# Kernel optimization log

Measured on AMD Instinct MI355X. Metric: run time of the kernel, lower is better.

The kernel has to match this reference:

```python
import jax, jax.numpy as jnp
import numpy as np
import math

B, S, D, H, R = 4, 2048, 512, 8, 8  # R = k+1 relative slots per direction


def setup_inputs() -> dict:
    key = jax.random.key(0)
    ks = jax.random.split(key, 16)
    dk = D // H
    sc = 1.0 / math.sqrt(D)
    return {
        "query": jax.random.normal(ks[0], (B, S, D), jnp.float32),
        "key": jax.random.normal(ks[1], (B, S, D), jnp.float32),
        "value": jax.random.normal(ks[2], (B, S, D), jnp.float32),
        "start_nodes": jax.random.randint(ks[3], (B, H, R, S), 0, S, jnp.int64 if jax.config.jax_enable_x64 else jnp.int32),
        "end_nodes": jax.random.randint(ks[4], (B, H, R, S), 0, S, jnp.int64 if jax.config.jax_enable_x64 else jnp.int32),
        "rel_q": jax.random.normal(ks[5], (1, H, 2 * R, dk), jnp.float32),
        "rel_k": jax.random.normal(ks[6], (1, H, 2 * R, dk), jnp.float32),
        "rel_v": jax.random.normal(ks[7], (1, H, 2 * R, dk), jnp.float32),
        "Wq": jax.random.normal(ks[8], (D, D), jnp.float32) * sc,
        "bq": jnp.zeros((D,), jnp.float32),
        "Wk": jax.random.normal(ks[9], (D, D), jnp.float32) * sc,
        "bk": jnp.zeros((D,), jnp.float32),
        "Wv": jax.random.normal(ks[10], (D, D), jnp.float32) * sc,
        "bv": jnp.zeros((D,), jnp.float32),
        "Wo": jax.random.normal(ks[11], (D, D), jnp.float32) * sc,
        "bo": jnp.zeros((D,), jnp.float32),
    }


def reference(query, key, value, start_nodes, end_nodes, rel_q, rel_k, rel_v,
              Wq, bq, Wk, bk, Wv, bv, Wo, bo):
    Bs, Ss, Ds = query.shape
    Hs = start_nodes.shape[1]
    dk = Ds // Hs

    def proj(x, W, b):
        return (x @ W.T + b).reshape(Bs, Ss, Hs, dk).transpose(0, 2, 1, 3)  # [B,H,S,dk]

    q = proj(query, Wq, bq)
    k = proj(key, Wk, bk)
    v = proj(value, Wv, bv)

    start_mask = start_nodes == -1
    sn = jnp.where(start_mask, 0, start_nodes)  # -1 padding -> 0 (masked out below)
    qidx = jnp.concatenate([end_nodes, sn], axis=2)  # [B,H,2R,S]
    kidx = jnp.concatenate([sn, end_nodes], axis=2)

    bi = jnp.arange(Bs)[:, None, None, None]
    hi = jnp.arange(Hs)[None, :, None, None]
    q_ctx = q[bi, hi, qidx]  # [B,H,2R,S,dk]
    k_ctx = k[bi, hi, kidx]
    v_ctx = v[bi, hi, kidx]

    # c2c + c2p + p2c, scale_factor = 3 (rel_q and rel_k both provided)
    scores = ((q_ctx * k_ctx).sum(-1)
              + (q_ctx * rel_k[:, :, :, None, :]).sum(-1)
              + (rel_q[:, :, :, None, :] * k_ctx).sum(-1))
    scores = scores / (3.0 * jnp.sqrt(jnp.asarray(dk, scores.dtype)))

    # mask: padded edges masked in both halves; first S flat entries always masked
    mask = jnp.concatenate([start_mask, start_mask], axis=2).reshape(Bs, Hs, -1)
    mask = mask.at[:, :, :Ss].set(True)
    sflat = jnp.exp(jnp.where(mask, -1e9, scores.reshape(Bs, Hs, -1)))  # [B,H,2R*S]

    qf = qidx.reshape(Bs, Hs, -1)
    b2 = jnp.arange(Bs)[:, None, None]
    h2 = jnp.arange(Hs)[None, :, None]
    # scatter-add softmax denominator over destination nodes, then gather back
    denom = jnp.zeros((Bs, Hs, Ss), sflat.dtype).at[b2, h2, qf].add(sflat)
    denom = jnp.where(denom == 0, -1e9, denom)
    probs = (sflat / denom[b2, h2, qf]).reshape(Bs, Hs, -1, Ss, 1)  # [B,H,2R,S,1]

    attn_v = probs * (v_ctx + rel_v[:, :, :, None, :])  # [B,H,2R,S,dk]
    out = jnp.zeros((Bs, Hs, Ss, dk), attn_v.dtype).at[b2, h2, qf].add(
        attn_v.reshape(Bs, Hs, -1, dk))  # scatter-add aggregation over edges

    out = out.transpose(0, 2, 1, 3).reshape(Bs, Ss, Ds)
    return out @ Wo.T + bo
```

## Files before the change

kernel.cpp:

```cpp
#include <hip/hip_runtime.h>
#include <math.h>

#define B_ 4
#define S_ 2048
#define D_ 512
#define H_ 8
#define R_ 8
#define DK_ 64
#define NEDGE (B_*H_*2*R_*S_)
#define EPB   (2*R_*S_)
#define ELLCAP 64
#define ELLSTRIDE 72
#define SCALE_ (1.0f/24.0f)

typedef __attribute__((ext_vector_type(8))) short bf16x8;
typedef __attribute__((ext_vector_type(8))) unsigned short ushort8_t;
typedef __attribute__((ext_vector_type(4))) float f32x4;

#define AS1q const __attribute__((address_space(1)))
#define AS3q __attribute__((address_space(3)))

__device__ inline unsigned short f2bf(float f) {
    unsigned u = __builtin_bit_cast(unsigned, f);
    u += 0x7fffu + ((u >> 16) & 1u);
    return (unsigned short)(u >> 16);
}
__device__ inline float bf2f(unsigned short u) {
    return __builtin_bit_cast(float, ((unsigned)u) << 16);
}

__global__ __launch_bounds__(256) void prep(
    const float* __restrict__ query, const float* __restrict__ key,
    const float* __restrict__ value,
    const float* __restrict__ Wq, const float* __restrict__ Wk,
    const float* __restrict__ Wv, const float* __restrict__ Wo,
    unsigned short* __restrict__ qc, unsigned short* __restrict__ kc,
    unsigned short* __restrict__ vc,
    unsigned short* __restrict__ wqb, unsigned short* __restrict__ wkb,
    unsigned short* __restrict__ wvb, unsigned short* __restrict__ wob)
{
    int bid = blockIdx.x;
    const float* x;
    unsigned short* y;
    size_t i;
    if (bid < 12288) {
        int z = bid >> 12;
        x = (z == 0) ? query : (z == 1) ? key : value;
        y = (z == 0) ? qc : (z == 1) ? kc : vc;
        i = ((size_t)(bid & 4095) * 256 + threadIdx.x) * 4;
    } else {
        int r = bid - 12288;
        int z = r >> 8;
        x = (z == 0) ? Wq : (z == 1) ? Wk : (z == 2) ? Wv : Wo;
        y = (z == 0) ? wqb : (z == 1) ? wkb : (z == 2) ? wvb : wob;
        i = ((size_t)(r & 255) * 256 + threadIdx.x) * 4;
    }
    float4 v = *(const float4*)&x[i];
    *(ushort4*)&y[i] = make_ushort4(f2bf(v.x), f2bf(v.y), f2bf(v.z), f2bf(v.w));
}

template<int TN>
__global__ __launch_bounds__(256) void gemm_bf16(
    const unsigned short* __restrict__ A0, const unsigned short* __restrict__ A1,
    const unsigned short* __restrict__ A2,
    const unsigned short* __restrict__ W0, const unsigned short* __restrict__ W1,
    const unsigned short* __restrict__ W2,
    const float* __restrict__ bi0, const float* __restrict__ bi1, const float* __restrict__ bi2,
    unsigned short* __restrict__ C0, unsigned short* __restrict__ C1,
    unsigned short* __restrict__ C2,
    float* __restrict__ Cf, int a_bhsd)
{
    constexpr int NFR = TN / 32;
    __shared__ unsigned short As[128 * 64];
    __shared__ unsigned short Bs[TN * 64];
    const int z = blockIdx.z;
    const unsigned short* A = (z == 0) ? A0 : (z == 1) ? A1 : A2;
    const unsigned short* W = (z == 0) ? W0 : (z == 1) ? W1 : W2;
    const float* bias        = (z == 0) ? bi0 : (z == 1) ? bi1 : bi2;
    unsigned short* C        = (z == 0) ? C0 : (z == 1) ? C1 : C2;

    const int t    = threadIdx.x;
    const int lane = t & 63;
    const int w    = t >> 6;
    const int wm   = w >> 1, wn = w & 1;
    const int m0   = blockIdx.x * 128;
    const int n0   = blockIdx.y * TN;

    const int lr    = lane >> 3;
    const int cglob = (lane & 7) ^ lr;

    f32x4 acc[4][NFR] = {};

    for (int kk = 0; kk < D_; kk += 64) {
        #pragma unroll
        for (int i = 0; i < 4; ++i) {
            int rowl = w * 32 + i * 8;
            int m = m0 + rowl + lr;
            const unsigned short* ga;
            if (a_bhsd) {
                int b = m >> 11, s = m & (S_ - 1), h = kk >> 6;
                ga = A + ((((size_t)b * H_ + h) * S_ + s) << 6) + cglob * 8;
            } else {
                ga = A + (size_t)m * D_ + kk + cglob * 8;
            }
            __builtin_amdgcn_global_load_lds((AS1q unsigned*)ga,
                (AS3q unsigned*)(As + rowl * 64), 16, 0, 0);
        }
        #pragma unroll
        for (int i = 0; i < TN / 32; ++i) {
            int rowl = w * (TN / 4) + i * 8;
            const unsigned short* gb =
                W + (size_t)(n0 + rowl + lr) * D_ + kk + cglob * 8;
            __builtin_amdgcn_global_load_lds((AS1q unsigned*)gb,
                (AS3q unsigned*)(Bs + rowl * 64), 16, 0, 0);
        }
        __syncthreads();

        #pragma unroll
        for (int ks = 0; ks < 64; ks += 32) {
            const int c0 = ks >> 3;
            bf16x8 af[4], bfr[NFR];
            #pragma unroll
            for (int mi = 0; mi < 4; ++mi) {
                int row = wm * 64 + mi * 16 + (lane & 15);
                int cp  = (c0 + (lane >> 4)) ^ (lane & 7);
                af[mi] = *(const bf16x8*)&As[row * 64 + cp * 8];
            }
            #pragma unroll
            for (int nj = 0; nj < NFR; ++nj) {
                int row = wn * (TN / 2) + nj * 16 + (lane & 15);
                int cp  = (c0 + (lane >> 4)) ^ (lane & 7);
                bfr[nj] = *(const bf16x8*)&Bs[row * 64 + cp * 8];
            }
            #pragma unroll
            for (int mi = 0; mi < 4; ++mi)
                #pragma unroll
                for (int nj = 0; nj < NFR; ++nj)
                    acc[mi][nj] = __builtin_amdgcn_mfma_f32_16x16x32_bf16(af[mi], bfr[nj], acc[mi][nj], 0, 0, 0);
        }
        __syncthreads();
    }

    #pragma unroll
    for (int mi = 0; mi < 4; ++mi) {
        #pragma unroll
        for (int nj = 0; nj < NFR; ++nj) {
            #pragma unroll
            for (int r = 0; r < 4; ++r) {
                int m = m0 + wm * 64 + mi * 16 + (lane >> 4) * 4 + r;
                int n = n0 + wn * (TN / 2) + nj * 16 + (lane & 15);
                float val = acc[mi][nj][r] + bias[n];
                if (Cf) {
                    Cf[(size_t)m * D_ + n] = val;
                } else {
                    int b = m >> 11, s = m & (S_ - 1);
                    int h = n >> 6,  d = n & 63;
                    C[((((size_t)b * H_ + h) * S_ + s) << 6) + d] = f2bf(val);
                }
            }
        }
    }
}

__global__ __launch_bounds__(256) void rel_dots(
    const unsigned short* __restrict__ q, const unsigned short* __restrict__ k_,
    const float* __restrict__ rel_q, const float* __restrict__ rel_k,
    float* __restrict__ qrk, float* __restrict__ rqk)
{
    const int t    = threadIdx.x;
    const int lane = t & 63;
    const int w    = t >> 6;
    const int n0   = blockIdx.x * 128 + w * 32;
    const int h    = (n0 >> 11) & 7;
    const int r2   = lane & 15;
    const int ch   = lane >> 4;

    bf16x8 bk2[2], bq2[2];
    #pragma unroll
    for (int ks = 0; ks < 2; ++ks) {
        const float* pk = rel_k + (((h << 4) + r2) << 6) + ks * 32 + ch * 8;
        const float* pq = rel_q + (((h << 4) + r2) << 6) + ks * 32 + ch * 8;
        f32x4 k0 = *(const f32x4*)pk, k1 = *(const f32x4*)(pk + 4);
        f32x4 q0 = *(const f32x4*)pq, q1 = *(const f32x4*)(pq + 4);
        bf16x8 bk, bq;
        #pragma unroll
        for (int i = 0; i < 4; ++i) {
            bk[i]     = (short)f2bf(k0[i]);
            bk[4 + i] = (short)f2bf(k1[i]);
            bq[i]     = (short)f2bf(q0[i]);
            bq[4 + i] = (short)f2bf(q1[i]);
        }
        bk2[ks] = bk; bq2[ks] = bq;
    }

    f32x4 aq[2] = {{0.f,0.f,0.f,0.f},{0.f,0.f,0.f,0.f}};
    f32x4 ak[2] = {{0.f,0.f,0.f,0.f},{0.f,0.f,0.f,0.f}};
    #pragma unroll
    for (int mi = 0; mi < 2; ++mi) {
        int m = n0 + mi * 16 + r2;
        #pragma unroll
        for (int ks = 0; ks < 2; ++ks) {
            bf16x8 aqf = *(const bf16x8*)&q [((size_t)m << 6) + ks * 32 + ch * 8];
            bf16x8 akf = *(const bf16x8*)&k_[((size_t)m << 6) + ks * 32 + ch * 8];
            aq[mi] = __builtin_amdgcn_mfma_f32_16x16x32_bf16(aqf, bk2[ks], aq[mi], 0, 0, 0);
            ak[mi] = __builtin_amdgcn_mfma_f32_16x16x32_bf16(akf, bq2[ks], ak[mi], 0, 0, 0);
        }
    }
    #pragma unroll
    for (int mi = 0; mi < 2; ++mi) {
        #pragma unroll
        for (int r = 0; r < 4; ++r) {
            int m = n0 + mi * 16 + (ch << 2) + r;
            qrk[((size_t)m << 4) + r2] = aq[mi][r] * SCALE_;
            rqk[((size_t)m << 4) + r2] = ak[mi][r] * SCALE_;
        }
    }
}

__global__ __launch_bounds__(1024) void attn_fused(
    const unsigned short* __restrict__ q, const unsigned short* __restrict__ k_,
    const unsigned short* __restrict__ v_,
    const float* __restrict__ qrk, const float* __restrict__ rqk,
    const float* __restrict__ rel_v,
    const int* __restrict__ start_nodes, const int* __restrict__ end_nodes,
    unsigned short* __restrict__ attn)
{
    __shared__ unsigned short ell[128 * ELLSTRIDE];
    __shared__ int cnt[128];
    const int bi  = blockIdx.x;
    const int xcd = bi & 7;
    const int loc = bi >> 3;
    const int bh  = xcd * 4 + (loc >> 4);
    const int dlo = (loc & 15) << 7;
    const int t   = threadIdx.x;

    if (t < 128) cnt[t] = 0;
    __syncthreads();

    const int base_idx = bh * (R_ * S_);
    for (int f = S_ + t * 2; f < EPB; f += 2048) {
        int r2 = f >> 11;
        int s  = f & (S_ - 1);
        int idx = base_idx + ((r2 & 7) << 11) + s;
        int2 sn2 = *(const int2*)&start_nodes[idx];
        int2 en2 = *(const int2*)&end_nodes[idx];
        #pragma unroll
        for (int u = 0; u < 2; ++u) {
            int sn = u ? sn2.y : sn2.x;
            if (sn == -1) continue;
            int en = u ? en2.y : en2.x;
            int dst = (r2 < R_) ? en : sn;
            unsigned rel = (unsigned)(dst - dlo);
            if (rel < 128u) {
                int ki = (r2 < R_) ? sn : en;
                int pos = atomicAdd(&cnt[rel], 1);
                if (pos < ELLCAP)
                    ell[rel * ELLSTRIDE + pos] = (unsigned short)((r2 << 11) | ki);
            }
        }
    }
    __syncthreads();

    const int w    = t >> 6;
    const int lane = t & 63;
    const int g    = lane >> 3;
    const int sub  = lane & 7;
    const int dl   = w * 8 + g;
    const int dst  = dlo + dl;
    const int h    = bh & 7;
    const size_t node_base = ((size_t)bh << 11);
    const float* qrk_bh = qrk + (node_base << 4);
    const float* rqk_bh = rqk + (node_base << 4);
    const float* rvh    = rel_v + ((size_t)(h << 4) << 6);

    ushort8_t q8 = *(const ushort8_t*)&q[((node_base + dst) << 6) + sub * 8];
    float qv[8];
    #pragma unroll
    for (int i = 0; i < 8; ++i) qv[i] = bf2f(q8[i]);
    const float* qrow = qrk_bh + ((size_t)dst << 4);

    int n = cnt[dl];
    if (n > ELLCAP) n = ELLCAP;
    int nmax = n;
    nmax = max(nmax, __shfl_xor(nmax, 8));
    nmax = max(nmax, __shfl_xor(nmax, 16));
    nmax = max(nmax, __shfl_xor(nmax, 32));

    const unsigned short* er = &ell[dl * ELLSTRIDE];

    float den = 0.f;
    float o[8] = {};

    int d0 = er[0];
    int ki = (0 < n) ? (d0 & (S_ - 1)) : 0;
    int r2 = (0 < n) ? ((d0 >> 11) & 15) : 0;
    ushort8_t k8 = *(const ushort8_t*)&k_[((node_base + ki) << 6) + sub * 8];
    ushort8_t v8 = *(const ushort8_t*)&v_[((node_base + ki) << 6) + sub * 8];
    float tb = qrow[r2] + rqk_bh[((size_t)ki << 4) + r2];

    for (int j = 0; j < nmax; ++j) {
        bool vn = (j + 1) < n;
        int dn = er[j + 1];
        int kin = vn ? (dn & (S_ - 1)) : 0;
        int r2n = vn ? ((dn >> 11) & 15) : 0;
        ushort8_t k8n = *(const ushort8_t*)&k_[((node_base + kin) << 6) + sub * 8];
        ushort8_t v8n = *(const ushort8_t*)&v_[((node_base + kin) << 6) + sub * 8];
        float tbn = qrow[r2n] + rqk_bh[((size_t)kin << 4) + r2n];

        bool valid = j < n;
        float p = 0.f;
        #pragma unroll
        for (int i = 0; i < 8; ++i)
            p = fmaf(bf2f(k8[i]), qv[i], p);
        p += __shfl_xor(p, 1);
        p += __shfl_xor(p, 2);
        p += __shfl_xor(p, 4);
        float sf = valid ? __expf(fmaf(p, SCALE_, tb)) : 0.f;
        const float* rvp = rvh + (r2 << 6) + sub * 8;
        f32x4 rv0 = *(const f32x4*)rvp;
        f32x4 rv1 = *(const f32x4*)(rvp + 4);
        den += sf;
        #pragma unroll
        for (int i = 0; i < 4; ++i)
            o[i] = fmaf(sf, bf2f(v8[i]) + rv0[i], o[i]);
        #pragma unroll
        for (int i = 0; i < 4; ++i)
            o[4 + i] = fmaf(sf, bf2f(v8[4 + i]) + rv1[i], o[4 + i]);

        k8 = k8n; v8 = v8n; tb = tbn; r2 = r2n;
    }

    float inv = (den > 0.f) ? 1.0f / den : 0.f;
    ushort8_t r;
    #pragma unroll
    for (int i = 0; i < 8; ++i) r[i] = f2bf(o[i] * inv);
    *(ushort8_t*)&attn[((node_base + dst) << 6) + sub * 8] = r;
}

extern "C" void kernel_launch(void* const* d_in, const int* in_sizes, int n_in,
                              void* d_out, int out_size, void* d_ws, size_t ws_size,
                              hipStream_t stream) {
    const float* query = (const float*)d_in[0];
    const float* key   = (const float*)d_in[1];
    const float* value = (const float*)d_in[2];
    const int* start_nodes = (const int*)d_in[3];
    const int* end_nodes   = (const int*)d_in[4];
    const float* rel_q = (const float*)d_in[5];
    const float* rel_k = (const float*)d_in[6];
    const float* rel_v = (const float*)d_in[7];
    const float* Wq = (const float*)d_in[8];
    const float* bq = (const float*)d_in[9];
    const float* Wk = (const float*)d_in[10];
    const float* bk = (const float*)d_in[11];
    const float* Wv = (const float*)d_in[12];
    const float* bv = (const float*)d_in[13];
    const float* Wo = (const float*)d_in[14];
    const float* bo = (const float*)d_in[15];
    float* out = (float*)d_out;

    const size_t NQ = (size_t)B_ * H_ * S_ * DK_;
    const size_t NW = (size_t)D_ * D_;
    unsigned short* p = (unsigned short*)d_ws;
    unsigned short* qc = p;            p += NQ;
    unsigned short* kc = p;            p += NQ;
    unsigned short* vc = p;            p += NQ;
    unsigned short* q  = p;            p += NQ;
    unsigned short* k  = p;            p += NQ;
    unsigned short* v  = p;            p += NQ;
    unsigned short* attn = p;          p += NQ;
    unsigned short* wqb = p;           p += NW;
    unsigned short* wkb = p;           p += NW;
    unsigned short* wvb = p;           p += NW;
    unsigned short* wob = p;           p += NW;
    float* qrk = (float*)qc;
    float* rqk = qrk + ((size_t)1 << 20);

    prep<<<13312, 256, 0, stream>>>(query, key, value, Wq, Wk, Wv, Wo,
                                    qc, kc, vc, wqb, wkb, wvb, wob);

    dim3 ggrid(B_ * S_ / 128, D_ / 128, 3);
    gemm_bf16<128><<<ggrid, 256, 0, stream>>>(qc, kc, vc, wqb, wkb, wvb, bq, bk, bv,
                                              q, k, v, nullptr, 0);

    rel_dots<<<512, 256, 0, stream>>>(q, k, rel_q, rel_k, qrk, rqk);

    attn_fused<<<512, 1024, 0, stream>>>(q, k, v, qrk, rqk, rel_v,
                                         start_nodes, end_nodes, attn);

    dim3 ogrid(B_ * S_ / 128, D_ / 64, 1);
    gemm_bf16<64><<<ogrid, 256, 0, stream>>>(attn, attn, attn, wob, wob, wob, bo, bo, bo,
                                             nullptr, nullptr, nullptr, out, 1);
}
```

Measured before the change: 207.9 us.

## Precompute edge bias into LDS and double-depth prefetch K/V gathers

```diff
diff --git a/kernel.cpp b/kernel.cpp
--- a/kernel.cpp
+++ b/kernel.cpp
@@ -217,7 +217,7 @@
     }
 }
 
-__global__ __launch_bounds__(1024) void attn_fused(
+__global__ __launch_bounds__(1024, 8) void attn_fused(
     const unsigned short* __restrict__ q, const unsigned short* __restrict__ k_,
     const unsigned short* __restrict__ v_,
     const float* __restrict__ qrk, const float* __restrict__ rqk,
@@ -226,6 +226,7 @@
     unsigned short* __restrict__ attn)
 {
     __shared__ unsigned short ell[128 * ELLSTRIDE];
+    __shared__ float ell_tb[128 * ELLSTRIDE];
     __shared__ int cnt[128];
     const int bi  = blockIdx.x;
     const int xcd = bi & 7;
@@ -236,6 +237,10 @@
 
     if (t < 128) cnt[t] = 0;
     __syncthreads();
+
+    const size_t node_base = ((size_t)bh << 11);
+    const float* qrk_bh = qrk + (node_base << 4);
+    const float* rqk_bh = rqk + (node_base << 4);
 
     const int base_idx = bh * (R_ * S_);
     for (int f = S_ + t * 2; f < EPB; f += 2048) {
@@ -253,9 +258,13 @@
             unsigned rel = (unsigned)(dst - dlo);
             if (rel < 128u) {
                 int ki = (r2 < R_) ? sn : en;
+                float tb = qrk_bh[((size_t)dst << 4) + r2]
+                         + rqk_bh[((size_t)ki  << 4) + r2];
                 int pos = atomicAdd(&cnt[rel], 1);
-                if (pos < ELLCAP)
-                    ell[rel * ELLSTRIDE + pos] = (unsigned short)((r2 << 11) | ki);
+                if (pos < ELLCAP) {
+                    ell[rel * ELLSTRIDE + pos]    = (unsigned short)((r2 << 11) | ki);
+                    ell_tb[rel * ELLSTRIDE + pos] = tb;
+                }
             }
         }
     }
@@ -268,16 +277,12 @@
     const int dl   = w * 8 + g;
     const int dst  = dlo + dl;
     const int h    = bh & 7;
-    const size_t node_base = ((size_t)bh << 11);
-    const float* qrk_bh = qrk + (node_base << 4);
-    const float* rqk_bh = rqk + (node_base << 4);
-    const float* rvh    = rel_v + ((size_t)(h << 4) << 6);
+    const float* rvh = rel_v + ((size_t)(h << 4) << 6);
 
     ushort8_t q8 = *(const ushort8_t*)&q[((node_base + dst) << 6) + sub * 8];
     float qv[8];
     #pragma unroll
     for (int i = 0; i < 8; ++i) qv[i] = bf2f(q8[i]);
-    const float* qrow = qrk_bh + ((size_t)dst << 4);
 
     int n = cnt[dl];
     if (n > ELLCAP) n = ELLCAP;
@@ -286,28 +291,21 @@
     nmax = max(nmax, __shfl_xor(nmax, 16));
     nmax = max(nmax, __shfl_xor(nmax, 32));
 
-    const unsigned short* er = &ell[dl * ELLSTRIDE];
+    const unsigned short* er  = &ell[dl * ELLSTRIDE];
+    const float*          etb = &ell_tb[dl * ELLSTRIDE];
 
     float den = 0.f;
     float o[8] = {};
 
-    int d0 = er[0];
-    int ki = (0 < n) ? (d0 & (S_ - 1)) : 0;
-    int r2 = (0 < n) ? ((d0 >> 11) & 15) : 0;
-    ushort8_t k8 = *(const ushort8_t*)&k_[((node_base + ki) << 6) + sub * 8];
-    ushort8_t v8 = *(const ushort8_t*)&v_[((node_base + ki) << 6) + sub * 8];
-    float tb = qrow[r2] + rqk_bh[((size_t)ki << 4) + r2];
-
-    for (int j = 0; j < nmax; ++j) {
-        bool vn = (j + 1) < n;
-        int dn = er[j + 1];
-        int kin = vn ? (dn & (S_ - 1)) : 0;
-        int r2n = vn ? ((dn >> 11) & 15) : 0;
-        ushort8_t k8n = *(const ushort8_t*)&k_[((node_base + kin) << 6) + sub * 8];
-        ushort8_t v8n = *(const ushort8_t*)&v_[((node_base + kin) << 6) + sub * 8];
-        float tbn = qrow[r2n] + rqk_bh[((size_t)kin << 4) + r2n];
-
-        bool valid = j < n;
+    auto issue = [&](int j, ushort8_t& k8o, ushort8_t& v8o, float& tbo, int& r2o) {
+        int d  = er[j];
+        int ki = d & (S_ - 1);
+        r2o = (d >> 11) & 15;
+        k8o = *(const ushort8_t*)&k_[((node_base + ki) << 6) + sub * 8];
+        v8o = *(const ushort8_t*)&v_[((node_base + ki) << 6) + sub * 8];
+        tbo = (j < n) ? etb[j] : -1e30f;
+    };
+    auto compute = [&](ushort8_t k8, ushort8_t v8, float tb, int r2) {
         float p = 0.f;
         #pragma unroll
         for (int i = 0; i < 8; ++i)
@@ -315,7 +313,7 @@
         p += __shfl_xor(p, 1);
         p += __shfl_xor(p, 2);
         p += __shfl_xor(p, 4);
-        float sf = valid ? __expf(fmaf(p, SCALE_, tb)) : 0.f;
+        float sf = __expf(fmaf(p, SCALE_, tb));
         const float* rvp = rvh + (r2 << 6) + sub * 8;
         f32x4 rv0 = *(const f32x4*)rvp;
         f32x4 rv1 = *(const f32x4*)(rvp + 4);
@@ -326,8 +324,24 @@
         #pragma unroll
         for (int i = 0; i < 4; ++i)
             o[4 + i] = fmaf(sf, bf2f(v8[4 + i]) + rv1[i], o[4 + i]);
-
-        k8 = k8n; v8 = v8n; tb = tbn; r2 = r2n;
+    };
+
+    ushort8_t kA, vA, kB, vB;
+    float tbA, tbB;
+    int rA, rB;
+    issue(0, kA, vA, tbA, rA);
+    issue(1, kB, vB, tbB, rB);
+
+    for (int j = 0; j < nmax; j += 2) {
+        ushort8_t kC, vC, kD, vD;
+        float tbC, tbD;
+        int rC, rD;
+        issue(j + 2, kC, vC, tbC, rC);
+        issue(j + 3, kD, vD, tbD, rD);
+        compute(kA, vA, tbA, rA);
+        compute(kB, vB, tbB, rB);
+        kA = kC; vA = vC; tbA = tbC; rA = rC;
+        kB = kD; vB = vD; tbB = tbD; rB = rD;
     }
 
     float inv = (den > 0.f) ? 1.0f / den : 0.f;
```

Result: slower. 324.9 us (+56.3%).
